# Performance work log

Measured on AMD Instinct MI355X. Metric: run time of the kernel, lower is better.

The kernel has to match this reference:

```python
import jax, jax.numpy as jnp
import numpy as np

NUM_TOKENS = 16384
MODEL_DIM = 4096
MAX_EXPERTS = 128
INITIAL_EXPERTS = 64
THRESHOLD = 0.5  # rm_threshold


def setup_inputs() -> dict:
    key = jax.random.key(0)
    k1, k2 = jax.random.split(key)
    x = jax.random.normal(k1, (NUM_TOKENS, MODEL_DIM), dtype=jnp.float32)
    # Linear(model_dim, max_expert_num, bias=False).weight -> [E_max, D]
    wg_weight = jax.random.normal(k2, (MAX_EXPERTS, MODEL_DIM), dtype=jnp.float32) * (1.0 / np.sqrt(MODEL_DIM))
    # experts_mask: first `INITIAL_EXPERTS` active
    experts_mask = (jnp.arange(MAX_EXPERTS) < INITIAL_EXPERTS).astype(jnp.float32)
    return {"x": x, "wg_weight": wg_weight, "experts_mask": experts_mask}


def reference(x, wg_weight, experts_mask):
    # gate logits: [N, E_max]
    scores = jnp.einsum("nd,ed->ne", x, wg_weight)
    # mask inactive experts
    scores = jnp.where(experts_mask[None, :] == 0, jnp.float32(-1e9), scores)
    # fp32 softmax + epsilon (matches F.softmax(..., dtype=float32) + 1e-14)
    scores = jax.nn.softmax(scores.astype(jnp.float32), axis=-1) + 1e-14
    # sort descending along expert dim
    sorted_scores = -jnp.sort(-scores, axis=-1)
    cum_scores = jnp.cumsum(sorted_scores, axis=-1)
    # adaptive top-k: experts needed to accumulate THRESHOLD routing mass
    mask = (cum_scores - sorted_scores) < THRESHOLD
    top_k = mask.sum(axis=-1).astype(jnp.int32)
    active_experts = experts_mask.sum().astype(jnp.int32)
    top_k = jnp.minimum(top_k, active_experts)
    return scores.astype(x.dtype), top_k
```

## Files before the change

kernel.cpp:

```cpp
#include <hip/hip_runtime.h>
#include <hip/hip_bf16.h>
#include <stdint.h>

#define NTOK 16384
#define DDIM 4096
#define NEXP 128
#define BM 64
#define BK 64
#define NT (DDIM / BK)

typedef __attribute__((ext_vector_type(8))) short short8;
typedef __attribute__((ext_vector_type(4))) float f32x4;
typedef __attribute__((address_space(1))) const uint32_t gu32;
typedef __attribute__((address_space(3))) uint32_t lu32;

__device__ __forceinline__ void gload16(const void* g, void* l) {
    __builtin_amdgcn_global_load_lds((gu32*)g, (lu32*)l, 16, 0, 0);
}

__device__ __forceinline__ void split_bf16(float f, uint32_t& h, uint32_t& l) {
    uint32_t u = __float_as_uint(f);
    h = (u + 0x7FFFu + ((u >> 16) & 1u)) >> 16;
    float r = f - __uint_as_float(h << 16);
    uint32_t v = __float_as_uint(r);
    l = (v + 0x7FFFu + ((v >> 16) & 1u)) >> 16;
}

__global__ void prep_w(const float* __restrict__ w,
                       uint16_t* __restrict__ whi, uint16_t* __restrict__ wlo) {
    int i = (blockIdx.x * blockDim.x + threadIdx.x) * 4;
    float4 f = *(const float4*)(w + i);
    uint32_t h0, h1, h2, h3, l0, l1, l2, l3;
    split_bf16(f.x, h0, l0);
    split_bf16(f.y, h1, l1);
    split_bf16(f.z, h2, l2);
    split_bf16(f.w, h3, l3);
    uint2 hv = make_uint2(h0 | (h1 << 16), h2 | (h3 << 16));
    uint2 lv = make_uint2(l0 | (l1 << 16), l2 | (l3 << 16));
    *(uint2*)(whi + i) = hv;
    *(uint2*)(wlo + i) = lv;
}

__global__ __launch_bounds__(512, 1) void gemm_logits(
    const float* __restrict__ x,
    const uint16_t* __restrict__ whi, const uint16_t* __restrict__ wlo,
    float* __restrict__ S)
{
    __shared__ uint16_t sAh[2][BM * BK], sAl[2][BM * BK];
    __shared__ uint16_t sBh[2][NEXP * BK], sBl[2][NEXP * BK];

    const int tid  = threadIdx.x;
    const int lane = tid & 63;
    const int wave = tid >> 6;
    const int wr = wave >> 2;
    const int wc = wave & 3;
    const int q = lane >> 4;
    const int c = lane & 15;
    const int rxor = c & 7;
    const int m0 = blockIdx.x * BM;

    const int ar = tid >> 3, aj = tid & 7;
    const float* xp = x + (size_t)(m0 + ar) * DDIM + aj * 8;
    const int aoff = ar * BK + (aj ^ (ar & 7)) * 8;

    const int bjj = aj ^ (ar & 7);
    const size_t bgo0 = (size_t)ar * DDIM + bjj * 8;
    const size_t bgo1 = bgo0 + (size_t)64 * DDIM;
    const int bd0 = tid * 8, bd1 = (tid + 512) * 8;

    f32x4 acc[2][2];
    #pragma unroll
    for (int mt = 0; mt < 2; ++mt)
        #pragma unroll
        for (int nt = 0; nt < 2; ++nt)
            acc[mt][nt] = (f32x4){0.f, 0.f, 0.f, 0.f};

    const int rA0 = (wr * 32 + c) * BK;
    const int rB0 = (wc * 32 + c) * BK;

    auto stageB = [&](int nxt, int kn) {
        gload16(whi + bgo0 + kn, &sBh[nxt][bd0]);
        gload16(whi + bgo1 + kn, &sBh[nxt][bd1]);
        gload16(wlo + bgo0 + kn, &sBl[nxt][bd0]);
        gload16(wlo + bgo1 + kn, &sBl[nxt][bd1]);
    };

    auto writeA = [&](int nxt, float4 fa, float4 fb) {
        uint32_t h[8], l[8];
        split_bf16(fa.x, h[0], l[0]); split_bf16(fa.y, h[1], l[1]);
        split_bf16(fa.z, h[2], l[2]); split_bf16(fa.w, h[3], l[3]);
        split_bf16(fb.x, h[4], l[4]); split_bf16(fb.y, h[5], l[5]);
        split_bf16(fb.z, h[6], l[6]); split_bf16(fb.w, h[7], l[7]);
        uint4 hv = make_uint4(h[0] | (h[1] << 16), h[2] | (h[3] << 16),
                              h[4] | (h[5] << 16), h[6] | (h[7] << 16));
        uint4 lv = make_uint4(l[0] | (l[1] << 16), l[2] | (l[3] << 16),
                              l[4] | (l[5] << 16), l[6] | (l[7] << 16));
        *(uint4*)&sAh[nxt][aoff] = hv;
        *(uint4*)&sAl[nxt][aoff] = lv;
    };

    auto compute = [&](int cur) {
        #pragma unroll
        for (int ks = 0; ks < 2; ++ks) {
            const int off = ((((ks << 2) | q)) ^ rxor) << 3;
            short8 ah[2], alo[2], bh[2], blo[2];
            #pragma unroll
            for (int mt = 0; mt < 2; ++mt) {
                const int ro = rA0 + mt * 16 * BK + off;
                ah[mt]  = *(const short8*)&sAh[cur][ro];
                alo[mt] = *(const short8*)&sAl[cur][ro];
            }
            #pragma unroll
            for (int nt = 0; nt < 2; ++nt) {
                const int ro = rB0 + nt * 16 * BK + off;
                bh[nt]  = *(const short8*)&sBh[cur][ro];
                blo[nt] = *(const short8*)&sBl[cur][ro];
            }
            #pragma unroll
            for (int mt = 0; mt < 2; ++mt)
                #pragma unroll
                for (int nt = 0; nt < 2; ++nt) {
                    acc[mt][nt] = __builtin_amdgcn_mfma_f32_16x16x32_bf16(alo[mt], bh[nt],  acc[mt][nt], 0, 0, 0);
                    acc[mt][nt] = __builtin_amdgcn_mfma_f32_16x16x32_bf16(ah[mt],  blo[nt], acc[mt][nt], 0, 0, 0);
                    acc[mt][nt] = __builtin_amdgcn_mfma_f32_16x16x32_bf16(ah[mt],  bh[nt],  acc[mt][nt], 0, 0, 0);
                }
        }
    };

    stageB(0, 0);
    {
        float4 fa = *(const float4*)(xp);
        float4 fb = *(const float4*)(xp + 4);
        writeA(0, fa, fb);
    }
    __syncthreads();

    #pragma unroll 2
    for (int t = 0; t < NT - 1; ++t) {
        const int cur = t & 1, nxt = cur ^ 1;
        const int kn = (t + 1) * BK;
        stageB(nxt, kn);
        float4 fa = *(const float4*)(xp + kn);
        float4 fb = *(const float4*)(xp + kn + 4);
        compute(cur);
        writeA(nxt, fa, fb);
        __syncthreads();
    }
    compute((NT - 1) & 1);

    #pragma unroll
    for (int mt = 0; mt < 2; ++mt)
        #pragma unroll
        for (int nt = 0; nt < 2; ++nt) {
            const int e = wc * 32 + nt * 16 + c;
            #pragma unroll
            for (int r = 0; r < 4; ++r) {
                const int tok = m0 + wr * 32 + mt * 16 + q * 4 + r;
                S[(size_t)tok * NEXP + e] = acc[mt][nt][r];
            }
        }
}

__global__ __launch_bounds__(256) void postproc(
    float* __restrict__ S, const float* __restrict__ mask,
    float* __restrict__ topk_out)
{
    const int lane = threadIdx.x & 63;
    const int wave = threadIdx.x >> 6;
    const int t = blockIdx.x * 4 + wave;
    float* row = S + (size_t)t * NEXP;

    float s0 = row[lane], s1 = row[lane + 64];
    float mk0 = mask[lane], mk1 = mask[lane + 64];
    const bool a0 = (mk0 != 0.f), a1 = (mk1 != 0.f);

    float mx = fmaxf(a0 ? s0 : -3.0e38f, a1 ? s1 : -3.0e38f);
    #pragma unroll
    for (int off = 32; off; off >>= 1) mx = fmaxf(mx, __shfl_xor(mx, off));

    float p0 = a0 ? __expf(s0 - mx) : 0.f;
    float p1 = a1 ? __expf(s1 - mx) : 0.f;
    float sum = p0 + p1;
    #pragma unroll
    for (int off = 32; off; off >>= 1) sum += __shfl_xor(sum, off);

    const float inv = 1.0f / sum;
    const float sc0 = p0 * inv + 1e-14f;
    const float sc1 = p1 * inv + 1e-14f;
    row[lane]      = sc0;
    row[lane + 64] = sc1;

    const int active = __popcll(__ballot(a0)) + __popcll(__ballot(a1));

    float v0 = sc0, v1 = sc1;
    float cum = 0.f;
    int k = 0;
    while (cum < 0.5f && k < NEXP) {
        float mv = fmaxf(v0, v1);
        #pragma unroll
        for (int off = 32; off; off >>= 1) mv = fmaxf(mv, __shfl_xor(mv, off));
        cum += mv;
        ++k;
        unsigned long long b = __ballot(v0 == mv || v1 == mv);
        int first = __ffsll(b) - 1;
        if (lane == first) {
            if (v0 == mv) v0 = -1.f; else v1 = -1.f;
        }
    }
    int topk = k < active ? k : active;
    if (lane == 0) topk_out[t] = (float)topk;
}

extern "C" void kernel_launch(void* const* d_in, const int* in_sizes, int n_in,
                              void* d_out, int out_size, void* d_ws, size_t ws_size,
                              hipStream_t stream) {
    (void)in_sizes; (void)n_in; (void)out_size; (void)ws_size;
    const float* x    = (const float*)d_in[0];
    const float* w    = (const float*)d_in[1];
    const float* mask = (const float*)d_in[2];

    float* S    = (float*)d_out;
    float* topk = S + (size_t)NTOK * NEXP;

    uint16_t* whi = (uint16_t*)d_ws;
    uint16_t* wlo = whi + (size_t)NEXP * DDIM;

    hipLaunchKernelGGL(prep_w, dim3((NEXP * DDIM) / (256 * 4)), dim3(256), 0, stream,
                       w, whi, wlo);
    hipLaunchKernelGGL(gemm_logits, dim3(NTOK / BM), dim3(512), 0, stream,
                       x, whi, wlo, S);
    hipLaunchKernelGGL(postproc, dim3(NTOK / 4), dim3(256), 0, stream,
                       S, mask, topk);
}
```

Baseline: 421.2 us.

## Fuse softmax and adaptive top-k postprocessing into the GEMM epilogue

```diff
diff --git a/kernel.cpp b/kernel.cpp
--- a/kernel.cpp
+++ b/kernel.cpp
@@ -8,6 +8,7 @@
 #define BM 64
 #define BK 64
 #define NT (DDIM / BK)
+#define SCP 132
 
 typedef __attribute__((ext_vector_type(8))) short short8;
 typedef __attribute__((ext_vector_type(4))) float f32x4;
@@ -41,13 +42,18 @@
     *(uint2*)(wlo + i) = lv;
 }
 
-__global__ __launch_bounds__(512, 1) void gemm_logits(
+__global__ __launch_bounds__(512, 1) void gemm_fused(
     const float* __restrict__ x,
     const uint16_t* __restrict__ whi, const uint16_t* __restrict__ wlo,
-    float* __restrict__ S)
+    const float* __restrict__ mask,
+    float* __restrict__ S, float* __restrict__ topk_out)
 {
-    __shared__ uint16_t sAh[2][BM * BK], sAl[2][BM * BK];
-    __shared__ uint16_t sBh[2][NEXP * BK], sBl[2][NEXP * BK];
+    __shared__ __align__(16) uint8_t smem[96 * 1024];
+    uint16_t* sAh = (uint16_t*)smem;
+    uint16_t* sAl = (uint16_t*)(smem + 16384);
+    uint16_t* sBh = (uint16_t*)(smem + 32768);
+    uint16_t* sBl = (uint16_t*)(smem + 65536);
+    float*    ssc = (float*)smem;
 
     const int tid  = threadIdx.x;
     const int lane = tid & 63;
@@ -79,10 +85,10 @@
     const int rB0 = (wc * 32 + c) * BK;
 
     auto stageB = [&](int nxt, int kn) {
-        gload16(whi + bgo0 + kn, &sBh[nxt][bd0]);
-        gload16(whi + bgo1 + kn, &sBh[nxt][bd1]);
-        gload16(wlo + bgo0 + kn, &sBl[nxt][bd0]);
-        gload16(wlo + bgo1 + kn, &sBl[nxt][bd1]);
+        gload16(whi + bgo0 + kn, &sBh[nxt * NEXP * BK + bd0]);
+        gload16(whi + bgo1 + kn, &sBh[nxt * NEXP * BK + bd1]);
+        gload16(wlo + bgo0 + kn, &sBl[nxt * NEXP * BK + bd0]);
+        gload16(wlo + bgo1 + kn, &sBl[nxt * NEXP * BK + bd1]);
     };
 
     auto writeA = [&](int nxt, float4 fa, float4 fb) {
@@ -95,26 +101,27 @@
                               h[4] | (h[5] << 16), h[6] | (h[7] << 16));
         uint4 lv = make_uint4(l[0] | (l[1] << 16), l[2] | (l[3] << 16),
                               l[4] | (l[5] << 16), l[6] | (l[7] << 16));
-        *(uint4*)&sAh[nxt][aoff] = hv;
-        *(uint4*)&sAl[nxt][aoff] = lv;
+        *(uint4*)&sAh[nxt * BM * BK + aoff] = hv;
+        *(uint4*)&sAl[nxt * BM * BK + aoff] = lv;
     };
 
     auto compute = [&](int cur) {
+        const int aB = cur * BM * BK, bB = cur * NEXP * BK;
         #pragma unroll
         for (int ks = 0; ks < 2; ++ks) {
             const int off = ((((ks << 2) | q)) ^ rxor) << 3;
             short8 ah[2], alo[2], bh[2], blo[2];
             #pragma unroll
             for (int mt = 0; mt < 2; ++mt) {
-                const int ro = rA0 + mt * 16 * BK + off;
-                ah[mt]  = *(const short8*)&sAh[cur][ro];
-                alo[mt] = *(const short8*)&sAl[cur][ro];
+                const int ro = aB + rA0 + mt * 16 * BK + off;
+                ah[mt]  = *(const short8*)&sAh[ro];
+                alo[mt] = *(const short8*)&sAl[ro];
             }
             #pragma unroll
             for (int nt = 0; nt < 2; ++nt) {
-                const int ro = rB0 + nt * 16 * BK + off;
-                bh[nt]  = *(const short8*)&sBh[cur][ro];
-                blo[nt] = *(const short8*)&sBl[cur][ro];
+                const int ro = bB + rB0 + nt * 16 * BK + off;
+                bh[nt]  = *(const short8*)&sBh[ro];
+                blo[nt] = *(const short8*)&sBl[ro];
             }
             #pragma unroll
             for (int mt = 0; mt < 2; ++mt)
@@ -147,6 +154,7 @@
         __syncthreads();
     }
     compute((NT - 1) & 1);
+    __syncthreads();
 
     #pragma unroll
     for (int mt = 0; mt < 2; ++mt)
@@ -155,60 +163,57 @@
             const int e = wc * 32 + nt * 16 + c;
             #pragma unroll
             for (int r = 0; r < 4; ++r) {
-                const int tok = m0 + wr * 32 + mt * 16 + q * 4 + r;
-                S[(size_t)tok * NEXP + e] = acc[mt][nt][r];
+                const int tr = wr * 32 + mt * 16 + q * 4 + r;
+                ssc[tr * SCP + e] = acc[mt][nt][r];
             }
         }
-}
-
-__global__ __launch_bounds__(256) void postproc(
-    float* __restrict__ S, const float* __restrict__ mask,
-    float* __restrict__ topk_out)
-{
-    const int lane = threadIdx.x & 63;
-    const int wave = threadIdx.x >> 6;
-    const int t = blockIdx.x * 4 + wave;
-    float* row = S + (size_t)t * NEXP;
-
-    float s0 = row[lane], s1 = row[lane + 64];
-    float mk0 = mask[lane], mk1 = mask[lane + 64];
+    __syncthreads();
+
+    const float mk0 = mask[lane];
+    const float mk1 = mask[lane + 64];
     const bool a0 = (mk0 != 0.f), a1 = (mk1 != 0.f);
-
-    float mx = fmaxf(a0 ? s0 : -3.0e38f, a1 ? s1 : -3.0e38f);
-    #pragma unroll
-    for (int off = 32; off; off >>= 1) mx = fmaxf(mx, __shfl_xor(mx, off));
-
-    float p0 = a0 ? __expf(s0 - mx) : 0.f;
-    float p1 = a1 ? __expf(s1 - mx) : 0.f;
-    float sum = p0 + p1;
-    #pragma unroll
-    for (int off = 32; off; off >>= 1) sum += __shfl_xor(sum, off);
-
-    const float inv = 1.0f / sum;
-    const float sc0 = p0 * inv + 1e-14f;
-    const float sc1 = p1 * inv + 1e-14f;
-    row[lane]      = sc0;
-    row[lane + 64] = sc1;
-
     const int active = __popcll(__ballot(a0)) + __popcll(__ballot(a1));
 
-    float v0 = sc0, v1 = sc1;
-    float cum = 0.f;
-    int k = 0;
-    while (cum < 0.5f && k < NEXP) {
-        float mv = fmaxf(v0, v1);
-        #pragma unroll
-        for (int off = 32; off; off >>= 1) mv = fmaxf(mv, __shfl_xor(mv, off));
-        cum += mv;
-        ++k;
-        unsigned long long b = __ballot(v0 == mv || v1 == mv);
-        int first = __ffsll(b) - 1;
-        if (lane == first) {
-            if (v0 == mv) v0 = -1.f; else v1 = -1.f;
+    for (int tt = 0; tt < 8; ++tt) {
+        const int tr = wave * 8 + tt;
+        const int tok = m0 + tr;
+        float s0 = ssc[tr * SCP + lane];
+        float s1 = ssc[tr * SCP + 64 + lane];
+
+        float mx = fmaxf(a0 ? s0 : -3.0e38f, a1 ? s1 : -3.0e38f);
+        #pragma unroll
+        for (int off = 32; off; off >>= 1) mx = fmaxf(mx, __shfl_xor(mx, off));
+
+        float p0 = a0 ? __expf(s0 - mx) : 0.f;
+        float p1 = a1 ? __expf(s1 - mx) : 0.f;
+        float sum = p0 + p1;
+        #pragma unroll
+        for (int off = 32; off; off >>= 1) sum += __shfl_xor(sum, off);
+
+        const float inv = 1.0f / sum;
+        const float sc0 = p0 * inv + 1e-14f;
+        const float sc1 = p1 * inv + 1e-14f;
+        S[(size_t)tok * NEXP + lane]      = sc0;
+        S[(size_t)tok * NEXP + lane + 64] = sc1;
+
+        float v0 = sc0, v1 = sc1;
+        float cum = 0.f;
+        int k = 0;
+        while (cum < 0.5f && k < NEXP) {
+            float mv = fmaxf(v0, v1);
+            #pragma unroll
+            for (int off = 32; off; off >>= 1) mv = fmaxf(mv, __shfl_xor(mv, off));
+            cum += mv;
+            ++k;
+            unsigned long long b = __ballot(v0 == mv || v1 == mv);
+            int first = __ffsll(b) - 1;
+            if (lane == first) {
+                if (v0 == mv) v0 = -1.f; else v1 = -1.f;
+            }
         }
+        int topk = k < active ? k : active;
+        if (lane == 0) topk_out[tok] = (float)topk;
     }
-    int topk = k < active ? k : active;
-    if (lane == 0) topk_out[t] = (float)topk;
 }
 
 extern "C" void kernel_launch(void* const* d_in, const int* in_sizes, int n_in,
@@ -227,8 +232,6 @@
 
     hipLaunchKernelGGL(prep_w, dim3((NEXP * DDIM) / (256 * 4)), dim3(256), 0, stream,
                        w, whi, wlo);
-    hipLaunchKernelGGL(gemm_logits, dim3(NTOK / BM), dim3(512), 0, stream,
-                       x, whi, wlo, S);
-    hipLaunchKernelGGL(postproc, dim3(NTOK / 4), dim3(256), 0, stream,
-                       S, mask, topk);
-}
+    hipLaunchKernelGGL(gemm_fused, dim3(NTOK / BM), dim3(512), 0, stream,
+                       x, whi, wlo, mask, S, topk);
+}
```

Result: slower. 445.5 us (+5.8%).

## Shrink GEMM tile to 32 tokens with 4 waves; pack 4 tokens per wave in postproc

Applied to the files above, without the earlier changes.

```diff
diff --git a/kernel.cpp b/kernel.cpp
--- a/kernel.cpp
+++ b/kernel.cpp
@@ -5,7 +5,7 @@
 #define NTOK 16384
 #define DDIM 4096
 #define NEXP 128
-#define BM 64
+#define BM 32
 #define BK 64
 #define NT (DDIM / BK)
 
@@ -41,7 +41,7 @@
     *(uint2*)(wlo + i) = lv;
 }
 
-__global__ __launch_bounds__(512, 1) void gemm_logits(
+__global__ __launch_bounds__(256) void gemm_logits(
     const float* __restrict__ x,
     const uint16_t* __restrict__ whi, const uint16_t* __restrict__ wlo,
     float* __restrict__ S)
@@ -52,8 +52,6 @@
     const int tid  = threadIdx.x;
     const int lane = tid & 63;
     const int wave = tid >> 6;
-    const int wr = wave >> 2;
-    const int wc = wave & 3;
     const int q = lane >> 4;
     const int c = lane & 15;
     const int rxor = c & 7;
@@ -64,9 +62,8 @@
     const int aoff = ar * BK + (aj ^ (ar & 7)) * 8;
 
     const int bjj = aj ^ (ar & 7);
-    const size_t bgo0 = (size_t)ar * DDIM + bjj * 8;
-    const size_t bgo1 = bgo0 + (size_t)64 * DDIM;
-    const int bd0 = tid * 8, bd1 = (tid + 512) * 8;
+    const size_t bgo = (size_t)ar * DDIM + bjj * 8;
+    const int bd = tid * 8;
 
     f32x4 acc[2][2];
     #pragma unroll
@@ -75,14 +72,13 @@
         for (int nt = 0; nt < 2; ++nt)
             acc[mt][nt] = (f32x4){0.f, 0.f, 0.f, 0.f};
 
-    const int rA0 = (wr * 32 + c) * BK;
-    const int rB0 = (wc * 32 + c) * BK;
-
     auto stageB = [&](int nxt, int kn) {
-        gload16(whi + bgo0 + kn, &sBh[nxt][bd0]);
-        gload16(whi + bgo1 + kn, &sBh[nxt][bd1]);
-        gload16(wlo + bgo0 + kn, &sBl[nxt][bd0]);
-        gload16(wlo + bgo1 + kn, &sBl[nxt][bd1]);
+        #pragma unroll
+        for (int rr = 0; rr < 4; ++rr) {
+            const size_t go = bgo + (size_t)rr * 32 * DDIM + kn;
+            gload16(whi + go, &sBh[nxt][bd + rr * 2048]);
+            gload16(wlo + go, &sBl[nxt][bd + rr * 2048]);
+        }
     };
 
     auto writeA = [&](int nxt, float4 fa, float4 fb) {
@@ -102,17 +98,17 @@
     auto compute = [&](int cur) {
         #pragma unroll
         for (int ks = 0; ks < 2; ++ks) {
-            const int off = ((((ks << 2) | q)) ^ rxor) << 3;
+            const int off = (((ks << 2) | q) ^ rxor) << 3;
             short8 ah[2], alo[2], bh[2], blo[2];
             #pragma unroll
             for (int mt = 0; mt < 2; ++mt) {
-                const int ro = rA0 + mt * 16 * BK + off;
+                const int ro = (mt * 16 + c) * BK + off;
                 ah[mt]  = *(const short8*)&sAh[cur][ro];
                 alo[mt] = *(const short8*)&sAl[cur][ro];
             }
             #pragma unroll
             for (int nt = 0; nt < 2; ++nt) {
-                const int ro = rB0 + nt * 16 * BK + off;
+                const int ro = (wave * 32 + nt * 16 + c) * BK + off;
                 bh[nt]  = *(const short8*)&sBh[cur][ro];
                 blo[nt] = *(const short8*)&sBl[cur][ro];
             }
@@ -152,10 +148,10 @@
     for (int mt = 0; mt < 2; ++mt)
         #pragma unroll
         for (int nt = 0; nt < 2; ++nt) {
-            const int e = wc * 32 + nt * 16 + c;
+            const int e = wave * 32 + nt * 16 + c;
             #pragma unroll
             for (int r = 0; r < 4; ++r) {
-                const int tok = m0 + wr * 32 + mt * 16 + q * 4 + r;
+                const int tok = m0 + mt * 16 + q * 4 + r;
                 S[(size_t)tok * NEXP + e] = acc[mt][nt][r];
             }
         }
@@ -167,48 +163,75 @@
 {
     const int lane = threadIdx.x & 63;
     const int wave = threadIdx.x >> 6;
-    const int t = blockIdx.x * 4 + wave;
-    float* row = S + (size_t)t * NEXP;
-
-    float s0 = row[lane], s1 = row[lane + 64];
-    float mk0 = mask[lane], mk1 = mask[lane + 64];
-    const bool a0 = (mk0 != 0.f), a1 = (mk1 != 0.f);
-
-    float mx = fmaxf(a0 ? s0 : -3.0e38f, a1 ? s1 : -3.0e38f);
-    #pragma unroll
-    for (int off = 32; off; off >>= 1) mx = fmaxf(mx, __shfl_xor(mx, off));
-
-    float p0 = a0 ? __expf(s0 - mx) : 0.f;
-    float p1 = a1 ? __expf(s1 - mx) : 0.f;
-    float sum = p0 + p1;
-    #pragma unroll
-    for (int off = 32; off; off >>= 1) sum += __shfl_xor(sum, off);
+    const int g  = lane >> 4;
+    const int gl = lane & 15;
+    const int tok = blockIdx.x * 16 + wave * 4 + g;
+    float* row = S + (size_t)tok * NEXP;
+
+    float v[8];
+    bool act[8];
+    int cnt = 0;
+    #pragma unroll
+    for (int j = 0; j < 8; ++j) {
+        v[j] = row[gl + 16 * j];
+        act[j] = (mask[gl + 16 * j] != 0.f);
+        cnt += act[j] ? 1 : 0;
+    }
+    int active = cnt;
+    #pragma unroll
+    for (int off = 8; off; off >>= 1) active += __shfl_xor(active, off);
+
+    float mx = -3.0e38f;
+    #pragma unroll
+    for (int j = 0; j < 8; ++j) mx = fmaxf(mx, act[j] ? v[j] : -3.0e38f);
+    #pragma unroll
+    for (int off = 8; off; off >>= 1) mx = fmaxf(mx, __shfl_xor(mx, off));
+
+    float sum = 0.f;
+    #pragma unroll
+    for (int j = 0; j < 8; ++j) {
+        v[j] = act[j] ? __expf(v[j] - mx) : 0.f;
+        sum += v[j];
+    }
+    #pragma unroll
+    for (int off = 8; off; off >>= 1) sum += __shfl_xor(sum, off);
 
     const float inv = 1.0f / sum;
-    const float sc0 = p0 * inv + 1e-14f;
-    const float sc1 = p1 * inv + 1e-14f;
-    row[lane]      = sc0;
-    row[lane + 64] = sc1;
-
-    const int active = __popcll(__ballot(a0)) + __popcll(__ballot(a1));
-
-    float v0 = sc0, v1 = sc1;
+    #pragma unroll
+    for (int j = 0; j < 8; ++j) {
+        v[j] = v[j] * inv + 1e-14f;
+        row[gl + 16 * j] = v[j];
+    }
+
     float cum = 0.f;
     int k = 0;
-    while (cum < 0.5f && k < NEXP) {
-        float mv = fmaxf(v0, v1);
-        #pragma unroll
-        for (int off = 32; off; off >>= 1) mv = fmaxf(mv, __shfl_xor(mv, off));
-        cum += mv;
-        ++k;
-        unsigned long long b = __ballot(v0 == mv || v1 == mv);
-        int first = __ffsll(b) - 1;
-        if (lane == first) {
-            if (v0 == mv) v0 = -1.f; else v1 = -1.f;
+    bool done = false;
+    while (__ballot(!done)) {
+        if (!done) {
+            float mv = v[0];
+            #pragma unroll
+            for (int j = 1; j < 8; ++j) mv = fmaxf(mv, v[j]);
+            #pragma unroll
+            for (int off = 8; off; off >>= 1) mv = fmaxf(mv, __shfl_xor(mv, off));
+            cum += mv;
+            ++k;
+            bool has = false;
+            #pragma unroll
+            for (int j = 0; j < 8; ++j) has |= (v[j] == mv);
+            unsigned int m16 = (unsigned int)((__ballot(has) >> (g * 16)) & 0xFFFFull);
+            int first = __ffs(m16) - 1;
+            if (gl == first) {
+                bool cleared = false;
+                #pragma unroll
+                for (int j = 0; j < 8; ++j) {
+                    if (!cleared && v[j] == mv) { v[j] = -1.f; cleared = true; }
+                }
+            }
+            done = (cum >= 0.5f) || (k >= NEXP);
         }
     }
     int topk = k < active ? k : active;
-    if (lane == 0) topk_out[t] = (float)topk;
+    if (gl == 0) topk_out[tok] = (float)topk;
 }
 
 extern "C" void kernel_launch(void* const* d_in, const int* in_sizes, int n_in,
@@ -227,8 +250,8 @@
 
     hipLaunchKernelGGL(prep_w, dim3((NEXP * DDIM) / (256 * 4)), dim3(256), 0, stream,
                        w, whi, wlo);
-    hipLaunchKernelGGL(gemm_logits, dim3(NTOK / BM), dim3(512), 0, stream,
+    hipLaunchKernelGGL(gemm_logits, dim3(NTOK / BM), dim3(256), 0, stream,
                        x, whi, wlo, S);
-    hipLaunchKernelGGL(postproc, dim3(NTOK / 4), dim3(256), 0, stream,
+    hipLaunchKernelGGL(postproc, dim3(NTOK / 16), dim3(256), 0, stream,
                        S, mask, topk);
 }
```

Result: no change. 425.8 us (+1.1%).
